# Optimization experiments

Measured on AMD Instinct MI355X. Metric: run time of the kernel, lower is better.

Reference implementation:

```python
import jax, jax.numpy as jnp
import numpy as np

C = 32           # in_channels
KH, KW = 3, 3    # kernel_range
SHIFT = 1
NP = KH * KW


def conv2d(x, w, b, pad):
    # x: NCHW, w: OIHW
    y = jax.lax.conv_general_dilated(
        x, w, window_strides=(1, 1), padding=[(pad, pad), (pad, pad)],
        dimension_numbers=('NCHW', 'OIHW', 'NCHW'))
    return y + b[None, :, None, None]


def setup_inputs() -> dict:
    key = jax.random.key(0)
    ks = jax.random.split(key, 14)
    p = lambda k, shape: (jax.random.normal(k, shape, dtype=jnp.float32) * 0.02)
    inp = {
        'x':  jax.random.normal(ks[0], (4, C, 256, 256), dtype=jnp.float32),
        'wk': p(ks[1], (C * NP, C, 1, 1)), 'bk': p(ks[2], (C * NP,)),
        'wv': p(ks[3], (C * NP, C, 1, 1)), 'bv': p(ks[4], (C * NP,)),
        'wq': p(ks[5], (C, C, 1, 1)),      'bq': p(ks[6], (C,)),
        'w1': p(ks[7], (C, C, 3, 3)),      'b1': p(ks[8], (C,)),
        'w2': p(ks[9], (2 * C, C, 3, 3)),  'b2': p(ks[10], (2 * C,)),
        'w3': p(ks[11], (C, 2 * C, 3, 3)), 'b3': p(ks[12], (C,)),
    }
    return inp


def reference(x, wk, bk, wv, bv, wq, bq, w1, b1, w2, b2, w3, b3):
    B, D, H, W = x.shape
    h_half, w_half = KH // 2, KW // 2
    ph, pw = h_half * SHIFT, w_half * SHIFT

    x_k = conv2d(x, wk, bk, 0)  # (B, D*NP, H, W)
    x_v = conv2d(x, wv, bv, 0)
    x_q = conv2d(x, wq, bq, 0)  # (B, D, H, W)

    pad4 = ((0, 0), (0, 0), (ph, ph), (pw, pw))
    x_k = jnp.pad(x_k, pad4)
    x_v = jnp.pad(x_v, pad4)
    mask_pad = jnp.pad(jnp.ones((B, 1, H, W), x.dtype), pad4)

    k_ls, v_ls, m_ls = [], [], []
    layer = 0
    for i in range(-h_half, h_half + 1):
        for j in range(-w_half, w_half + 1):
            r0 = ph + i * SHIFT
            c0 = pw + j * SHIFT
            k_ls.append(x_k[:, layer * D:(layer + 1) * D, r0:r0 + H, c0:c0 + W])
            v_ls.append(x_v[:, layer * D:(layer + 1) * D, r0:r0 + H, c0:c0 + W])
            m_ls.append(mask_pad[:, :, r0:r0 + H, c0:c0 + W])
            layer += 1

    # Faithful to torch .view semantics: flat row-major reshape, NOT a permute.
    k = jnp.stack(k_ls, axis=1).reshape(B * H * W, NP, D)   # (B,NP,D,H,W) -> flat
    v = jnp.stack(v_ls, axis=1).reshape(B * H * W, NP, D)
    m = jnp.stack(m_ls, axis=1).reshape(B * H * W, NP, 1)
    q = x_q.reshape(B * H * W, 1, D)                         # (B,D,H,W) -> flat

    scores = jnp.matmul(k, jnp.swapaxes(q, -1, -2)) * m / 8.0  # (N, NP, 1)
    alpha = jax.nn.softmax(scores, axis=1)
    res = jnp.matmul(jnp.swapaxes(alpha, -1, -2), v)           # (N, 1, D)
    t = res.reshape(B, D, H, W)

    t = jax.nn.relu(conv2d(t, w1, b1, 1))
    t = jax.nn.relu(conv2d(t, w2, b2, 1))
    t = jax.nn.relu(conv2d(t, w3, b3, 1))
    return t
```

## Files before the change

kernel.cpp:

```cpp
#include <hip/hip_runtime.h>
#include <hip/hip_bf16.h>

#define B_ 4
#define C_ 32
#define H_ 256
#define W_ 256
#define S_ 65536
#define NP_ 9
#define OC_ 288
#define PR 258
#define PWN 264

using bf16 = __hip_bfloat16;
typedef __attribute__((ext_vector_type(8)))  short  short8;
typedef __attribute__((ext_vector_type(4)))  short  short4_t;
typedef __attribute__((ext_vector_type(16))) float  f32x16;

__device__ __forceinline__ float b2f(short s) {
    return __uint_as_float(((unsigned)(unsigned short)s) << 16);
}

template<int IC, int OC>
__device__ __forceinline__ void prepA_body(int fid, const float* __restrict__ w,
                                           bf16* __restrict__ apk)
{
    constexpr int NK = 9 * IC / 16;
    int tile = fid >> 9;
    int l = (fid >> 3) & 63;
    int j = fid & 7;
    int mt = tile / NK;
    int ks = tile - mt * NK;
    int q = l >> 5;
    int oc = mt * 32 + (l & 31);
    int k = ks * 16 + q * 8 + j;
    int tap = k / IC;
    int ic = k - tap * IC;
    apk[fid] = __float2bfloat16(w[((oc * IC + ic) * 3 + tap / 3) * 3 + tap % 3]);
}

template<int G>
__device__ __forceinline__ void zerob_body(int b, int p, uint4* __restrict__ buf)
{
    int gran;
    if (p < 2 * PWN * G) {
        int row = (p < PWN * G) ? 0 : 257;
        int rem = p % (PWN * G);
        gran = row * PWN * G + rem;
    } else {
        int p2 = p - 2 * PWN * G;
        int col = (p2 < 256 * G) ? 0 : 257;
        int rem = p2 % (256 * G);
        int r = rem / G + 1;
        int icg = rem - (rem / G) * G;
        gran = (r * PWN + col) * G + icg;
    }
    buf[(size_t)b * PR * PWN * G + gran] = uint4{0, 0, 0, 0};
}

__global__ __launch_bounds__(256) void k_prep(
    const float* __restrict__ wk, const float* __restrict__ wv,
    const float* __restrict__ wq,
    const float* __restrict__ w1, const float* __restrict__ w2,
    const float* __restrict__ w3,
    bf16* __restrict__ apk0, bf16* __restrict__ apk1,
    bf16* __restrict__ apk2, bf16* __restrict__ apk3,
    uint4* __restrict__ tA, uint4* __restrict__ t1, uint4* __restrict__ t2)
{
    int idx = blockIdx.x * 256 + threadIdx.x;
    if (idx < 19456) {
        int j    = idx & 7;
        int lane = (idx >> 3) & 63;
        int ks   = (idx >> 9) & 1;
        int mt   = idx >> 10;
        int oc = lane & 31;
        int ic = ks * 16 + (lane >> 5) * 8 + j;
        const float* w; int ocg;
        if (mt < 9)       { w = wk; ocg = mt * 32 + oc; }
        else if (mt < 18) { w = wv; ocg = (mt - 9) * 32 + oc; }
        else              { w = wq; ocg = oc; }
        apk0[idx] = __float2bfloat16(w[ocg * C_ + ic]);
    } else if (idx < 28672) {
        prepA_body<32, 32>(idx - 19456, w1, apk1);
    } else if (idx < 47104) {
        prepA_body<32, 64>(idx - 28672, w2, apk2);
    } else if (idx < 65536) {
        prepA_body<64, 32>(idx - 47104, w3, apk3);
    } else if (idx < 82176) {
        int i5 = idx - 65536;
        zerob_body<4>(i5 / 4160, i5 % 4160, tA);
    } else if (idx < 98816) {
        int i6 = idx - 82176;
        zerob_body<4>(i6 / 4160, i6 % 4160, t1);
    } else if (idx < 132096) {
        int i7 = idx - 98816;
        zerob_body<8>(i7 / 8320, i7 % 8320, t2);
    }
}

__global__ __launch_bounds__(256) void k_q(
    const float* __restrict__ x, const bf16* __restrict__ apk,
    const float* __restrict__ bq, bf16* __restrict__ xq)
{
    __shared__ bf16 lbuf[32][140];
    int bh  = blockIdx.x >> 9;
    int blk = blockIdx.x & 511;
    int pixw0 = blk << 7;
    int tid  = threadIdx.x;
    int wvi  = tid >> 6;
    int lane = tid & 63;
    int col  = lane & 31, q = lane >> 5;
    int pix  = pixw0 + wvi * 32 + col;

    const float* xb = x + (size_t)bh * (C_ * S_);
    bf16* xqb = xq + (size_t)bh * (32 * S_);

    short8 bfrag[2];
#pragma unroll
    for (int kk = 0; kk < 2; ++kk)
#pragma unroll
        for (int j = 0; j < 8; ++j) {
            bf16 h = __float2bfloat16(xb[(size_t)(kk * 16 + q * 8 + j) * S_ + pix]);
            bfrag[kk][j] = *reinterpret_cast<short*>(&h);
        }

    const short8* apkv = reinterpret_cast<const short8*>(apk);
    f32x16 acc = {};
    acc = __builtin_amdgcn_mfma_f32_32x32x16_bf16(bfrag[0], apkv[(18 * 2 + 0) * 64 + lane], acc, 0, 0, 0);
    acc = __builtin_amdgcn_mfma_f32_32x32x16_bf16(bfrag[1], apkv[(18 * 2 + 1) * 64 + lane], acc, 0, 0, 0);
    float bbv = bq[col];
#pragma unroll
    for (int g4 = 0; g4 < 4; ++g4) {
        short4_t sv;
#pragma unroll
        for (int j = 0; j < 4; ++j) {
            bf16 hb = __float2bfloat16(acc[g4 * 4 + j] + bbv);
            sv[j] = *reinterpret_cast<short*>(&hb);
        }
        *reinterpret_cast<short4_t*>(&lbuf[col][wvi * 32 + 8 * g4 + 4 * q]) = sv;
    }
    __syncthreads();
    int ch0 = tid >> 4, chk = tid & 15, ch1 = ch0 + 16;
    short8 v0 = *reinterpret_cast<const short8*>(&lbuf[ch0][chk * 8]);
    *reinterpret_cast<short8*>(xqb + (size_t)ch0 * S_ + pixw0 + chk * 8) = v0;
    short8 v1 = *reinterpret_cast<const short8*>(&lbuf[ch1][chk * 8]);
    *reinterpret_cast<short8*>(xqb + (size_t)ch1 * S_ + pixw0 + chk * 8) = v1;
}


__device__ __forceinline__ void tile_store(char* __restrict__ kvB, int T, int q, int oc,
                                           const f32x16& a, float bias,
                                           int dj, int hb_lo, int hb_hi)
{
#pragma unroll
    for (int G2 = 0; G2 < 4; ++G2) {
        int pxb = 32 * T + 8 * G2 + 4 * q;
        bool hbad = (pxb < hb_lo) || (pxb >= hb_hi);
        short4_t sv;
#pragma unroll
        for (int j3 = 0; j3 < 4; ++j3) {
            int px = pxb + j3;
            bool wbad = (dj == 1 && (px & 255) == 255) || (dj == -1 && (px & 255) == 0);
            float val = (hbad || wbad) ? 0.f : (a[G2 * 4 + j3] + bias);
            bf16 h = __float2bfloat16(val);
            sv[j3] = *reinterpret_cast<short*>(&h);
        }
        *reinterpret_cast<short4_t*>(kvB + oc * 1616 +
            (((T << 2) + (G2 ^ ((oc >> 3) & 3))) << 4) + q * 8) = sv;
    }
}

#define CONV_TILE(T, VH, COND)                                                        \
    VH = (f32x16){};                                                                  \
    if (COND) {                                                                       \
        int xib = 32 * (T) + 257 + di * 256 + dj + col;                               \
        int swx = (xib ^ (xib >> 2)) & 3;                                             \
        short8 fa = *reinterpret_cast<const short8*>(&xs[xib * 4 + (q ^ swx)]);       \
        short8 fb = *reinterpret_cast<const short8*>(&xs[xib * 4 + ((2 + q) ^ swx)]); \
        f32x16 ka = (f32x16){};                                                       \
        ka = __builtin_amdgcn_mfma_f32_32x32x16_bf16(fa, apkv[(p * 2 + 0) * 64 + lane], ka, 0, 0, 0); \
        ka = __builtin_amdgcn_mfma_f32_32x32x16_bf16(fb, apkv[(p * 2 + 1) * 64 + lane], ka, 0, 0, 0); \
        VH = __builtin_amdgcn_mfma_f32_32x32x16_bf16(fa, apkv[((9 + p) * 2 + 0) * 64 + lane], VH, 0, 0, 0); \
        VH = __builtin_amdgcn_mfma_f32_32x32x16_bf16(fb, apkv[((9 + p) * 2 + 1) * 64 + lane], VH, 0, 0, 0); \
        tile_store(kvB, (T), q, col, ka, bK, dj, hb_lo, hb_hi);                       \
    }

#define V_TILE(T, VH, COND)                                                           \
    if (COND) tile_store(kvB, (T), q, col, VH, bV, dj, hb_lo, hb_hi);

__global__ __launch_bounds__(512, 2) void k_fused(
    const float* __restrict__ x,
    const bf16* __restrict__ apk,
    const float* __restrict__ bk, const float* __restrict__ bv,
    const bf16* __restrict__ xq,
    bf16* __restrict__ att)
{
    extern __shared__ char smem_raw[];
    uint4* xs  = reinterpret_cast<uint4*>(smem_raw);
    char*  kvB = smem_raw + 84096;

    int bb = blockIdx.x >> 7;
    int s0 = (blockIdx.x & 127) << 9;

    int tid  = threadIdx.x;
    int lane = tid & 63;
    int wv   = tid >> 6;
    int col  = lane & 31;
    int q    = lane >> 5;

    const float* xb = x + (size_t)bb * (C_ * S_);

    for (int i = tid; i < 5256; i += 512) {
        int xi = i >> 2, g = i & 3;
        int s = s0 - 257 + xi;
        short8 v;
        if ((unsigned)s < 65536u) {
#pragma unroll
            for (int j = 0; j < 8; ++j) {
                bf16 h = __float2bfloat16(xb[(size_t)(g * 8 + j) * S_ + s]);
                v[j] = *reinterpret_cast<short*>(&h);
            }
        } else {
#pragma unroll
            for (int j = 0; j < 8; ++j) v[j] = 0;
        }
        int sw = (xi ^ (xi >> 2)) & 3;
        *reinterpret_cast<short8*>(&xs[xi * 4 + (g ^ sw)]) = v;
    }
    __syncthreads();

    const short8* apkv = reinterpret_cast<const short8*>(apk);

    int grp  = tid >> 2, hh = tid & 3;
    int dp   = grp & 31;
    int krow = grp >> 5;
    size_t qbase = ((size_t)bb << 21);

#pragma unroll 1
    for (int p = 0; p < 9; ++p) {
        int di = p / 3 - 1, dj = p - (p / 3) * 3 - 1;
        int hb_lo = (di == -1) ? (256 - s0) : 0;
        int hb_hi = (di == 1) ? (65280 - s0) : 0x7FFFFFFF;
        float bK = bk[p * 32 + col];
        float bV = bv[p * 32 + col];

        f32x16 vh0, vh1, vh2, vh3;
        CONV_TILE(wv,      vh0, true)
        CONV_TILE(wv + 8,  vh1, true)
        CONV_TILE(wv + 16, vh2, true)
        CONV_TILE(wv + 24, vh3, (wv == 0))
        __syncthreads();

        int plane_base = (p * 32 + dp) << 16;
        int tl  = (plane_base + s0 + 287) / 288 + krow;
        int sk0 = tl * 288 - plane_base;
        bool rowvalid = (sk0 < s0 + 512) && (sk0 <= 65248);
        float wgt[9];
        float inv_ = 0.f;
        if (rowvalid) {
            float qv[8];
            short8 qg = *reinterpret_cast<const short8*>(xq + qbase + ((size_t)tl << 5) + hh * 8);
#pragma unroll
            for (int j = 0; j < 8; ++j) qv[j] = b2f(qg[j]);
            float sc[9];
#pragma unroll
            for (int seg = 0; seg < 9; ++seg) {
                int pxr = sk0 - s0 + seg * 32 + hh * 8;
                int t = pxr >> 5, G2r = (pxr >> 3) & 3;
                short8 kg = *reinterpret_cast<const short8*>(
                    kvB + dp * 1616 + (((t << 2) + (G2r ^ ((dp >> 3) & 3))) << 4));
                float dot = 0.f;
#pragma unroll
                for (int j = 0; j < 8; ++j) dot += qv[j] * b2f(kg[j]);
                dot += __shfl_xor(dot, 1);
                dot += __shfl_xor(dot, 2);
                int rm = tl * 9 + seg;
                int pm = rm >> 16, sm = rm & 65535;
                int dim = pm / 3 - 1, djm = pm - (pm / 3) * 3 - 1;
                int hm = sm >> 8, wm = sm & 255;
                bool mval = ((unsigned)(hm + dim) < 256u) && ((unsigned)(wm + djm) < 256u);
                sc[seg] = mval ? dot * 0.125f : 0.f;
            }
            float mx = sc[0];
#pragma unroll
            for (int s2 = 1; s2 < 9; ++s2) mx = fmaxf(mx, sc[s2]);
            float sum = 0.f;
#pragma unroll
            for (int s2 = 0; s2 < 9; ++s2) { wgt[s2] = __expf(sc[s2] - mx); sum += wgt[s2]; }
            inv_ = 1.f / sum;
        }
        __syncthreads();

        V_TILE(wv,      vh0, true)
        V_TILE(wv + 8,  vh1, true)
        V_TILE(wv + 16, vh2, true)
        V_TILE(wv + 24, vh3, (wv == 0))
        __syncthreads();

        if (rowvalid) {
            float oacc[8] = {0.f, 0.f, 0.f, 0.f, 0.f, 0.f, 0.f, 0.f};
#pragma unroll
            for (int seg = 0; seg < 9; ++seg) {
                int pxr = sk0 - s0 + seg * 32 + hh * 8;
                int t = pxr >> 5, G2r = (pxr >> 3) & 3;
                short8 vg = *reinterpret_cast<const short8*>(
                    kvB + dp * 1616 + (((t << 2) + (G2r ^ ((dp >> 3) & 3))) << 4));
                float w_ = wgt[seg];
#pragma unroll
                for (int j = 0; j < 8; ++j) oacc[j] += w_ * b2f(vg[j]);
            }
            short8 sv;
#pragma unroll
            for (int j = 0; j < 8; ++j) {
                bf16 h = __float2bfloat16(oacc[j] * inv_);
                sv[j] = *reinterpret_cast<short*>(&h);
            }
            *reinterpret_cast<short8*>(att + qbase + ((size_t)tl << 5) + hh * 8) = sv;
        }
        __syncthreads();
    }
}

__global__ __launch_bounds__(320) void k_strad(
    const float* __restrict__ x,
    const float* __restrict__ wk, const float* __restrict__ bk,
    const float* __restrict__ wv, const float* __restrict__ bv,
    const bf16* __restrict__ xq, bf16* __restrict__ att)
{
    __shared__ float kL[288], vL[288], qL[32], wgtL[10];
    int e = blockIdx.x;
    int b = e >> 8, i = e & 255;
    int g = i >> 3, u = i & 7;
    int tl = g * 2048 + (((2040 + u) * 1593) & 2047);
    int tid = threadIdx.x;

    if (tid < 288) {
        int f  = tl * 288 + tid;
        int cp = f >> 16;
        int sp = f & 65535;
        int tap = cp >> 5;
        int di = tap / 3 - 1, dj = tap - (tap / 3) * 3 - 1;
        int h = sp >> 8, w = sp & 255;
        bool valid = ((unsigned)(h + di) < 256u) && ((unsigned)(w + dj) < 256u);
        float kv_ = 0.f, vv_ = 0.f;
        if (valid) {
            int sx = sp + di * 256 + dj;
            const float* xp = x + (size_t)b * (C_ * S_) + sx;
            float ks = bk[cp], vs = bv[cp];
#pragma unroll
            for (int ic = 0; ic < 32; ++ic) {
                float xv_ = xp[(size_t)ic * S_];
                ks += wk[cp * 32 + ic] * xv_;
                vs += wv[cp * 32 + ic] * xv_;
            }
            kv_ = ks; vv_ = vs;
        }
        kL[tid] = kv_; vL[tid] = vv_;
    }
    if (tid < 32) {
        bf16 hv = xq[(size_t)b * (32 * S_) + (size_t)tl * 32 + tid];
        qL[tid] = b2f(*reinterpret_cast<short*>(&hv));
    }
    __syncthreads();
    if (tid < 9) {
        float dot = 0.f;
#pragma unroll
        for (int d = 0; d < 32; ++d) dot += kL[tid * 32 + d] * qL[d];
        int rm = tl * 9 + tid;
        int pm = rm >> 16, sm = rm & 65535;
        int dim = pm / 3 - 1, djm = pm - (pm / 3) * 3 - 1;
        int hm = sm >> 8, wm = sm & 255;
        bool mval = ((unsigned)(hm + dim) < 256u) && ((unsigned)(wm + djm) < 256u);
        wgtL[tid] = mval ? dot * 0.125f : 0.f;
    }
    __syncthreads();
    if (tid == 0) {
        float mx = wgtL[0];
#pragma unroll
        for (int s2 = 1; s2 < 9; ++s2) mx = fmaxf(mx, wgtL[s2]);
        float sum = 0.f;
#pragma unroll
        for (int s2 = 0; s2 < 9; ++s2) { wgtL[s2] = __expf(wgtL[s2] - mx); sum += wgtL[s2]; }
        wgtL[9] = 1.f / sum;
    }
    __syncthreads();
    if (tid < 32) {
        float acc = 0.f;
#pragma unroll
        for (int seg = 0; seg < 9; ++seg) acc += wgtL[seg] * vL[seg * 32 + tid];
        att[(size_t)b * 2097152 + (size_t)tl * 32 + tid] = __float2bfloat16(acc * wgtL[9]);
    }
}

__global__ __launch_bounds__(256) void k_repack(
    const bf16* __restrict__ att, bf16* __restrict__ tA)
{
    int idx = blockIdx.x * 256 + threadIdx.x;
    int icg = idx & 3;
    int ps  = idx >> 2;
    int b = ps >> 16;
    int s = ps & 65535;
    const bf16* src = att + (size_t)b * (32 * S_) + icg * 8 * S_ + s;
    short8 v;
#pragma unroll
    for (int j = 0; j < 8; ++j)
        v[j] = *reinterpret_cast<const short*>(src + (size_t)j * S_);
    int row = (s >> 8) + 1, colp = (s & 255) + 1;
    *reinterpret_cast<short8*>(tA + ((size_t)((b * PR + row) * PWN + colp)) * 32 + icg * 8) = v;
}

template<int IC, int OC, bool NCHW_OUT>
__global__ __launch_bounds__(256) void k_conv3s(
    const bf16* __restrict__ in,
    const bf16* __restrict__ apk,
    const float* __restrict__ bs,
    void* __restrict__ outv)
{
    constexpr int G    = IC / 8;
    constexpr int M    = OC / 32;
    constexpr int KPT  = IC / 16;
    constexpr int NK   = 9 * KPT;
    constexpr int NT   = 2;
    constexpr int ROWP = 66;
    constexpr int ROWG = ROWP * G;
    constexpr int TOTG = 6 * ROWG;

    __shared__ uint4 smem[TOTG];

    int wg   = blockIdx.x;
    int orig = (wg & 7) * 128 + (wg >> 3);
    int b   = orig >> 8;
    int rem = orig & 255;
    int h0  = (rem >> 2) << 2;
    int w0  = (rem & 3) * 64;

    int tid = threadIdx.x;

    {
        const uint4* src = reinterpret_cast<const uint4*>(in);
#pragma unroll
        for (int i = 0; i < (TOTG + 255) / 256; ++i) {
            int idx = tid + i * 256;
            if (idx < TOTG) {
                int dr = idx / ROWG;
                int r2 = idx - dr * ROWG;
                uint4 v = src[((size_t)(b * PR + h0 + dr) * PWN + w0) * G + r2];
                int px = r2 >> ((G == 4) ? 2 : 3);
                int sw = (G == 4) ? ((px ^ (px >> 2)) & 3) : (px & 7);
                smem[dr * ROWG + (r2 & ~(G - 1)) + ((r2 ^ sw) & (G - 1))] = v;
            }
        }
    }
    __syncthreads();

    int lane = tid & 63;
    int wid  = tid >> 6;
    int col  = lane & 31, q = lane >> 5;
    int h    = h0 + wid;

    const short8* apkv = reinterpret_cast<const short8*>(apk);

    f32x16 acc[NT][M];
#pragma unroll
    for (int nt = 0; nt < NT; ++nt)
#pragma unroll
        for (int mt = 0; mt < M; ++mt) acc[nt][mt] = (f32x16){};

#pragma unroll
    for (int tap = 0; tap < 9; ++tap) {
        int dr = tap / 3 + wid;
        int dj = tap % 3;
#pragma unroll
        for (int icq = 0; icq < KPT; ++icq) {
            short8 bfr[NT];
#pragma unroll
            for (int nt = 0; nt < NT; ++nt) {
                int px = nt * 32 + col + dj;
                int sw = (G == 4) ? ((px ^ (px >> 2)) & 3) : (px & 7);
                bfr[nt] = *reinterpret_cast<const short8*>(
                    &smem[dr * ROWG + px * G + ((icq * 2 + q) ^ sw)]);
            }
#pragma unroll
            for (int mt = 0; mt < M; ++mt) {
                short8 afr = apkv[(mt * NK + tap * KPT + icq) * 64 + lane];
#pragma unroll
                for (int nt = 0; nt < NT; ++nt)
                    acc[nt][mt] = __builtin_amdgcn_mfma_f32_32x32x16_bf16(
                        afr, bfr[nt], acc[nt][mt], 0, 0, 0);
            }
        }
    }

#pragma unroll
    for (int nt = 0; nt < NT; ++nt) {
        int wout = w0 + nt * 32 + col;
#pragma unroll
        for (int mt = 0; mt < M; ++mt) {
            if (NCHW_OUT) {
                float* out = (float*)outv;
#pragma unroll
                for (int r = 0; r < 16; ++r) {
                    int oc = mt * 32 + (r & 3) + 8 * (r >> 2) + 4 * q;
                    out[(size_t)((b * OC + oc) * H_ + h) * W_ + wout] =
                        fmaxf(acc[nt][mt][r] + bs[oc], 0.f);
                }
            } else {
                bf16* out = (bf16*)outv;
                size_t base = (size_t)((b * PR + h + 1) * PWN + wout + 1) * OC + mt * 32 + 4 * q;
#pragma unroll
                for (int g4 = 0; g4 < 4; ++g4) {
                    short4_t sv;
#pragma unroll
                    for (int r4 = 0; r4 < 4; ++r4) {
                        int oc = mt * 32 + 8 * g4 + 4 * q + r4;
                        bf16 hh = __float2bfloat16(fmaxf(acc[nt][mt][g4 * 4 + r4] + bs[oc], 0.f));
                        sv[r4] = *reinterpret_cast<short*>(&hh);
                    }
                    *reinterpret_cast<short4_t*>(out + base + 8 * g4) = sv;
                }
            }
        }
    }
}

extern "C" void kernel_launch(void* const* d_in, const int* in_sizes, int n_in,
                              void* d_out, int out_size, void* d_ws, size_t ws_size,
                              hipStream_t stream)
{
    const float* x  = (const float*)d_in[0];
    const float* wk = (const float*)d_in[1];
    const float* bk = (const float*)d_in[2];
    const float* wv = (const float*)d_in[3];
    const float* bv = (const float*)d_in[4];
    const float* wq = (const float*)d_in[5];
    const float* bq = (const float*)d_in[6];
    const float* w1 = (const float*)d_in[7];
    const float* b1 = (const float*)d_in[8];
    const float* w2 = (const float*)d_in[9];
    const float* b2 = (const float*)d_in[10];
    const float* w3 = (const float*)d_in[11];
    const float* b3 = (const float*)d_in[12];
    float* out = (float*)d_out;
    char* ws = (char*)d_ws;

    bf16* xq   = (bf16*)(ws);
    bf16* tA   = (bf16*)(ws + 16777216);
    bf16* t1   = (bf16*)(ws + 34213888);
    bf16* t2   = (bf16*)(ws + 51650560);
    bf16* apk0 = (bf16*)(ws + 86523904);
    bf16* apk1 = (bf16*)(ws + 86562816);
    bf16* apk2 = (bf16*)(ws + 86581248);
    bf16* apk3 = (bf16*)(ws + 86618112);
    bf16* attB = (bf16*)d_out;

    static bool attr_set = false;
    if (!attr_set) {
        hipFuncSetAttribute(reinterpret_cast<const void*>(k_fused),
                            hipFuncAttributeMaxDynamicSharedMemorySize, 135808);
        attr_set = true;
    }

    k_prep<<<516, 256, 0, stream>>>(wk, wv, wq, w1, w2, w3,
                                    apk0, apk1, apk2, apk3,
                                    (uint4*)tA, (uint4*)t1, (uint4*)t2);

    k_q<<<2048, 256, 0, stream>>>(x, apk0, bq, xq);

    k_fused<<<512, 512, 135808, stream>>>(x, apk0, bk, bv, xq, attB);

    k_strad<<<1024, 320, 0, stream>>>(x, wk, bk, wv, bv, xq, attB);

    k_repack<<<4096, 256, 0, stream>>>(attB, tA);

    k_conv3s<32, 32, false><<<1024, 256, 0, stream>>>(tA, apk1, b1, (void*)t1);
    k_conv3s<32, 64, false><<<1024, 256, 0, stream>>>(t1, apk2, b2, (void*)t2);
    k_conv3s<64, 32, true ><<<1024, 256, 0, stream>>>(t2, apk3, b3, (void*)out);
}
```

Measured before the change: 183.7 us.

## Double k_fused block to 1024 threads and split attention rows across more lanes

Launches k_fused with 1024 threads per block instead of 512. Each wave now computes two conv MFMA tiles per plane instead of four, and attention dot products use 4-element slices with one extra shuffle stage. Only the first 512 threads do the attention work. The q load is also hoisted ahead of the MFMA phase to hide its latency. The aim is more wave-level parallelism inside a block whose large shared-memory footprint limits occupancy. The cost is higher register pressure under the 1024-thread launch bound and half the threads idling during attention.

```diff
diff --git a/kernel.cpp b/kernel.cpp
--- a/kernel.cpp
+++ b/kernel.cpp
@@ -14,6 +14,7 @@
 using bf16 = __hip_bfloat16;
 typedef __attribute__((ext_vector_type(8)))  short  short8;
 typedef __attribute__((ext_vector_type(4)))  short  short4_t;
+typedef __attribute__((ext_vector_type(2)))  short  short2_t;
 typedef __attribute__((ext_vector_type(16))) float  f32x16;
 
 __device__ __forceinline__ float b2f(short s) {
@@ -187,7 +188,7 @@
 #define V_TILE(T, VH, COND)                                                           \
     if (COND) tile_store(kvB, (T), q, col, VH, bV, dj, hb_lo, hb_hi);
 
-__global__ __launch_bounds__(512, 2) void k_fused(
+__global__ __launch_bounds__(1024, 4) void k_fused(
     const float* __restrict__ x,
     const bf16* __restrict__ apk,
     const float* __restrict__ bk, const float* __restrict__ bv,
@@ -209,7 +210,7 @@
 
     const float* xb = x + (size_t)bb * (C_ * S_);
 
-    for (int i = tid; i < 5256; i += 512) {
+    for (int i = tid; i < 5256; i += 1024) {
         int xi = i >> 2, g = i & 3;
         int s = s0 - 257 + xi;
         short8 v;
@@ -226,14 +227,18 @@
         int sw = (xi ^ (xi >> 2)) & 3;
         *reinterpret_cast<short8*>(&xs[xi * 4 + (g ^ sw)]) = v;
     }
+
+    const short8* apkv = reinterpret_cast<const short8*>(apk);
+
+    int grp  = tid >> 3, sub = tid & 7;
+    int dp   = grp & 31;
+    int krow = (grp >> 5) & 1;
+    int hh   = sub >> 1;
+    int sh   = sub & 1;
+    bool athr = tid < 512;
+    size_t qbase = ((size_t)bb << 21);
+
     __syncthreads();
-
-    const short8* apkv = reinterpret_cast<const short8*>(apk);
-
-    int grp  = tid >> 2, hh = tid & 3;
-    int dp   = grp & 31;
-    int krow = grp >> 5;
-    size_t qbase = ((size_t)bb << 21);
 
 #pragma unroll 1
     for (int p = 0; p < 9; ++p) {
@@ -243,36 +248,41 @@
         float bK = bk[p * 32 + col];
         float bV = bv[p * 32 + col];
 
-        f32x16 vh0, vh1, vh2, vh3;
+        int tl = 0, sk0 = 0; bool rv = false;
+        short4_t qg = {};
+        if (athr) {
+            int plane_base = (p * 32 + dp) << 16;
+            tl  = (plane_base + s0 + 287) / 288 + krow;
+            sk0 = tl * 288 - plane_base;
+            rv  = (sk0 < s0 + 512) && (sk0 <= 65248);
+            if (rv) qg = *reinterpret_cast<const short4_t*>(
+                         xq + qbase + ((size_t)tl << 5) + hh * 8 + sh * 4);
+        }
+
+        f32x16 vh0, vh1;
         CONV_TILE(wv,      vh0, true)
-        CONV_TILE(wv + 8,  vh1, true)
-        CONV_TILE(wv + 16, vh2, true)
-        CONV_TILE(wv + 24, vh3, (wv == 0))
+        CONV_TILE(wv + 16, vh1, (wv < 9))
         __syncthreads();
 
-        int plane_base = (p * 32 + dp) << 16;
-        int tl  = (plane_base + s0 + 287) / 288 + krow;
-        int sk0 = tl * 288 - plane_base;
-        bool rowvalid = (sk0 < s0 + 512) && (sk0 <= 65248);
         float wgt[9];
         float inv_ = 0.f;
-        if (rowvalid) {
-            float qv[8];
-            short8 qg = *reinterpret_cast<const short8*>(xq + qbase + ((size_t)tl << 5) + hh * 8);
-#pragma unroll
-            for (int j = 0; j < 8; ++j) qv[j] = b2f(qg[j]);
+        if (rv) {
+            float qv[4];
+#pragma unroll
+            for (int j = 0; j < 4; ++j) qv[j] = b2f(qg[j]);
+            int swz = (dp >> 3) & 3;
+            int t0  = (sk0 - s0) >> 5;
             float sc[9];
 #pragma unroll
             for (int seg = 0; seg < 9; ++seg) {
-                int pxr = sk0 - s0 + seg * 32 + hh * 8;
-                int t = pxr >> 5, G2r = (pxr >> 3) & 3;
-                short8 kg = *reinterpret_cast<const short8*>(
-                    kvB + dp * 1616 + (((t << 2) + (G2r ^ ((dp >> 3) & 3))) << 4));
+                short4_t kg = *reinterpret_cast<const short4_t*>(
+                    kvB + dp * 1616 + ((((t0 + seg) << 2) + (hh ^ swz)) << 4) + sh * 8);
                 float dot = 0.f;
 #pragma unroll
-                for (int j = 0; j < 8; ++j) dot += qv[j] * b2f(kg[j]);
+                for (int j = 0; j < 4; ++j) dot += qv[j] * b2f(kg[j]);
                 dot += __shfl_xor(dot, 1);
                 dot += __shfl_xor(dot, 2);
+                dot += __shfl_xor(dot, 4);
                 int rm = tl * 9 + seg;
                 int pm = rm >> 16, sm = rm & 65535;
                 int dim = pm / 3 - 1, djm = pm - (pm / 3) * 3 - 1;
@@ -291,30 +301,28 @@
         __syncthreads();
 
         V_TILE(wv,      vh0, true)
-        V_TILE(wv + 8,  vh1, true)
-        V_TILE(wv + 16, vh2, true)
-        V_TILE(wv + 24, vh3, (wv == 0))
+        V_TILE(wv + 16, vh1, (wv < 9))
         __syncthreads();
 
-        if (rowvalid) {
-            float oacc[8] = {0.f, 0.f, 0.f, 0.f, 0.f, 0.f, 0.f, 0.f};
+        if (rv) {
+            int swz = (dp >> 3) & 3;
+            int t0  = (sk0 - s0) >> 5;
+            float oacc[4] = {0.f, 0.f, 0.f, 0.f};
 #pragma unroll
             for (int seg = 0; seg < 9; ++seg) {
-                int pxr = sk0 - s0 + seg * 32 + hh * 8;
-                int t = pxr >> 5, G2r = (pxr >> 3) & 3;
-                short8 vg = *reinterpret_cast<const short8*>(
-                    kvB + dp * 1616 + (((t << 2) + (G2r ^ ((dp >> 3) & 3))) << 4));
+                short4_t vg = *reinterpret_cast<const short4_t*>(
+                    kvB + dp * 1616 + ((((t0 + seg) << 2) + (hh ^ swz)) << 4) + sh * 8);
                 float w_ = wgt[seg];
 #pragma unroll
-                for (int j = 0; j < 8; ++j) oacc[j] += w_ * b2f(vg[j]);
-            }
-            short8 sv;
-#pragma unroll
-            for (int j = 0; j < 8; ++j) {
+                for (int j = 0; j < 4; ++j) oacc[j] += w_ * b2f(vg[j]);
+            }
+            short4_t sv;
+#pragma unroll
+            for (int j = 0; j < 4; ++j) {
                 bf16 h = __float2bfloat16(oacc[j] * inv_);
                 sv[j] = *reinterpret_cast<short*>(&h);
             }
-            *reinterpret_cast<short8*>(att + qbase + ((size_t)tl << 5) + hh * 8) = sv;
+            *reinterpret_cast<short4_t*>(att + qbase + ((size_t)tl << 5) + hh * 8 + sh * 4) = sv;
         }
         __syncthreads();
     }
@@ -565,7 +573,7 @@
 
     k_q<<<2048, 256, 0, stream>>>(x, apk0, bq, xq);
 
-    k_fused<<<512, 512, 135808, stream>>>(x, apk0, bk, bv, xq, attB);
+    k_fused<<<512, 1024, 135808, stream>>>(x, apk0, bk, bv, xq, attB);
 
     k_strad<<<1024, 320, 0, stream>>>(x, wk, bk, wv, bv, xq, attB);
 
```

Result: no change. 182.8 us (-0.5%).
